# Kernel tuning notes

Hardware: AMD Instinct MI355X
Metric: run time of the kernel (lower is better)

The kernel has to match this reference:

```python
import jax, jax.numpy as jnp
import numpy as np

D = 32          # embedding_size
B = 16384       # batch_size
P = 16          # neighbor_sample_size (paths per item per hop)
NE = 100000     # n_entity
NU = 100000     # n_user
NR = 32         # n_relation
N_ITER = 2


def setup_inputs() -> dict:
    key = jax.random.key(0)
    ks = jax.random.split(key, 20)
    s = 0.1
    nrm = lambda k, sh: jax.random.normal(k, sh, dtype=jnp.float32) * s
    inp = {
        "user_table": nrm(ks[0], (NU, D)),
        "ent_table": nrm(ks[1], (NE, D)),
        "rel_table": nrm(ks[2], (NR, D)),
        # PyTorch LSTM params, gate order (i, f, g, o)
        "w_ih0": nrm(ks[3], (4 * D, 2 * D)),
        "w_hh0": nrm(ks[4], (4 * D, D)),
        "b_ih0": nrm(ks[5], (4 * D,)),
        "b_hh0": nrm(ks[6], (4 * D,)),
        "w_ih1": nrm(ks[7], (4 * D, 2 * D)),
        "w_hh1": nrm(ks[8], (4 * D, D)),
        "b_ih1": nrm(ks[9], (4 * D,)),
        "b_hh1": nrm(ks[10], (4 * D,)),
        "agg_w": nrm(ks[11], (D, D)),
        "agg_b": nrm(ks[12], (D,)),
        "users": jax.random.randint(ks[13], (B,), 0, NU),
        "items": jax.random.randint(ks[14], (B,), 0, NE),
        "ratings": jax.random.randint(ks[15], (B,), 0, 2),
        # hop h path table: [n_entity, P, 2*(h+1)+1]; values < 32 valid for both tables
        "lp0": jax.random.randint(ks[16], (NE, P, 3), 0, 32),
        "lp1": jax.random.randint(ks[17], (NE, P, 5), 0, 32),
    }
    return inp


def _lstm_last(seq, w_ih, w_hh, b_ih, b_hh):
    # seq: [N, T, 2D] -> final hidden state [N, D], PyTorch gate order i,f,g,o
    N = seq.shape[0]
    H = w_hh.shape[1]
    bias = b_ih + b_hh

    def step(carry, x):
        h, c = carry
        g = x @ w_ih.T + h @ w_hh.T + bias
        i, f, gg, o = jnp.split(g, 4, axis=-1)
        c = jax.nn.sigmoid(f) * c + jax.nn.sigmoid(i) * jnp.tanh(gg)
        h = jax.nn.sigmoid(o) * jnp.tanh(c)
        return (h, c), None

    h0 = jnp.zeros((N, H), seq.dtype)
    (h, _), _ = jax.lax.scan(step, (h0, h0), jnp.swapaxes(seq, 0, 1))
    return h


def _forward(user_table, ent_table, rel_table, lstm_params, agg_w, agg_b,
             users, items, ratings, lps):
    u = user_table[users]                # [B, D]
    items_emb = ent_table[items]         # [B, D]
    for hop in range(N_ITER):
        lp = lps[hop]
        w_ih, w_hh, b_ih, b_hh = lstm_params[hop]
        il = lp[items]                   # [B, P, 2*(hop+1)+1]
        seed_e = ent_table[il[:, :, 0]]  # [B, P, D]
        u_b = jnp.broadcast_to(u[:, None, :], seed_e.shape)
        first = jnp.concatenate([u_b, seed_e], -1)[:, :, None, :]   # [B,P,1,2D]
        rel_e = rel_table[il[:, :, 1::2]]                            # [B,P,hop+1,D]
        tail_e = ent_table[il[:, :, 2::2]]                           # [B,P,hop+1,D]
        rest = jnp.concatenate([rel_e, tail_e], -1)                  # [B,P,hop+1,2D]
        seq = jnp.concatenate([first, rest], 2).reshape(B * P, hop + 2, 2 * D)
        h = _lstm_last(seq, w_ih, w_hh, b_ih, b_hh)                  # [B*P, D]
        final = h.reshape(B, P, D).sum(axis=1)                       # hidden_out sum
        items_emb = (items_emb + final) @ agg_w.T + agg_b            # 'sum' aggregator
    scores = jnp.sum(u * items_emb, axis=-1)                         # [B]
    r = ratings.astype(scores.dtype)
    # stable BCE on sigmoid(scores)
    loss = -jnp.mean(r * jax.nn.log_sigmoid(scores) + (1.0 - r) * jax.nn.log_sigmoid(-scores))
    return loss, jax.nn.sigmoid(scores)


def reference(user_table, ent_table, rel_table,
              w_ih0, w_hh0, b_ih0, b_hh0,
              w_ih1, w_hh1, b_ih1, b_hh1,
              agg_w, agg_b,
              users, items, ratings, lp0, lp1):
    lstm_params = [(w_ih0, w_hh0, b_ih0, b_hh0), (w_ih1, w_hh1, b_ih1, b_hh1)]
    loss, scores_normalized = _forward(user_table, ent_table, rel_table,
                                       lstm_params, agg_w, agg_b,
                                       users, items, ratings, (lp0, lp1))
    return (loss, scores_normalized, items)
```

## Files before the change

### kernel.cpp

```cpp
#include <hip/hip_runtime.h>
#include <math.h>

#define D  32
#define BN 16384
#define PP 16

typedef __bf16 bf16x8 __attribute__((ext_vector_type(8)));
typedef __bf16 bf16x4 __attribute__((ext_vector_type(4)));
typedef float  floatx4 __attribute__((ext_vector_type(4)));

#define K1 1.44269504088896341f
#define K2 2.88539008177792681f

#define WHH_OFF    0
#define T0T_OFF    10240
#define TRT_OFF    20480
#define IMG_BYTES  30720
#define H_OFF      30720
#define LDS_BYTES  (IMG_BYTES + 8 * 1280)

__device__ __forceinline__ float sigf(float x) {
    float e = __builtin_amdgcn_exp2f(-x * K1);
    return __builtin_amdgcn_rcpf(1.0f + e);
}
__device__ __forceinline__ float logsigf(float x) {
    float ax = fabsf(x);
    float l = log1pf(__expf(-ax));
    return (x >= 0.0f) ? -l : x - l;
}
__device__ __forceinline__ floatx4 cvt4(bf16x4 v) {
    floatx4 r = { (float)v[0], (float)v[1], (float)v[2], (float)v[3] };
    return r;
}

__device__ __forceinline__ bf16x8 onehot8(int sel, int q) {
    union { unsigned w[4]; bf16x8 v; } u;
    const unsigned val = 0x3F80u << ((sel & 1) * 16);
    const int grp = sel >> 1;
    #pragma unroll
    for (int wd = 0; wd < 4; ++wd)
        u.w[wd] = (grp == q * 4 + wd) ? val : 0u;
    return u.v;
}

__global__ __launch_bounds__(256)
void prep_tables(const float* __restrict__ user_table,
                 const float* __restrict__ ent, const float* __restrict__ rel,
                 const float* __restrict__ wih0, const float* __restrict__ whh0,
                 const float* __restrict__ bih0, const float* __restrict__ bhh0,
                 const float* __restrict__ wih1, const float* __restrict__ whh1,
                 const float* __restrict__ bih1, const float* __restrict__ bhh1,
                 const int* __restrict__ users, const int* __restrict__ items,
                 const int* __restrict__ lp0, const int* __restrict__ lp1,
                 char* __restrict__ imgs, __bf16* __restrict__ GU,
                 int* __restrict__ pidx)
{
    const int id = blockIdx.x * 256 + threadIdx.x;
    if (id < 8192) {
        const int hop  = id >> 12;
        const int e    = id & 4095;
        const int gate = e >> 5, d = e & 31;
        float v = (hop ? whh1 : whh0)[(size_t)gate * 32 + d];
        ((__bf16*)(imgs + hop * IMG_BYTES + WHH_OFF))[gate * 40 + d] = (__bf16)v;
    } else if (id < 16384) {
        const int idb = id - 8192;
        const int hop = idb >> 12;
        const int g   = (idb >> 5) & 127;
        const int k   = idb & 31;
        const float* wih = hop ? wih1 : wih0;
        const float4* w4 = (const float4*)(wih + (size_t)g * 64 + 32);
        const float4* e4 = (const float4*)(ent + (size_t)k * 32);
        float a = hop ? bih1[g] + bhh1[g] : bih0[g] + bhh0[g];
        #pragma unroll
        for (int i = 0; i < 8; ++i) {
            float4 w = w4[i], x = e4[i];
            a = fmaf(w.x, x.x, a); a = fmaf(w.y, x.y, a);
            a = fmaf(w.z, x.z, a); a = fmaf(w.w, x.w, a);
        }
        ((__bf16*)(imgs + hop * IMG_BYTES + T0T_OFF))[g * 40 + k] = (__bf16)a;
    } else if (id < 24576) {
        const int idb = id - 16384;
        const int hop = idb >> 12;
        const int g   = (idb >> 5) & 127;
        const int j   = idb & 31;
        const float* wih = hop ? wih1 : wih0;
        const float4* w4 = (const float4*)(wih + (size_t)g * 64);
        const float4* r4 = (const float4*)(rel + (size_t)j * 32);
        float a = 0.0f;
        #pragma unroll
        for (int i = 0; i < 8; ++i) {
            float4 w = w4[i], x = r4[i];
            a = fmaf(w.x, x.x, a); a = fmaf(w.y, x.y, a);
            a = fmaf(w.z, x.z, a); a = fmaf(w.w, x.w, a);
        }
        ((__bf16*)(imgs + hop * IMG_BYTES + TRT_OFF))[g * 40 + j] = (__bf16)a;
    } else if (id < 1073152) {
        const int c   = id - 24576;
        const int hop = c >> 19;
        const int gq  = (c >> 14) & 31;
        const int fb  = c & 16383;
        const float* wih = hop ? wih1 : wih0;
        const float4* u4 = (const float4*)(user_table + (size_t)users[fb] * 32);
        float4 uu[8];
        #pragma unroll
        for (int i = 0; i < 8; ++i) uu[i] = u4[i];
        __bf16 r[4];
        #pragma unroll
        for (int t = 0; t < 4; ++t) {
            const float4* w4 = (const float4*)(wih + (size_t)(gq * 4 + t) * 64);
            float a = 0.0f;
            #pragma unroll
            for (int i = 0; i < 8; ++i) {
                float4 w = w4[i];
                a = fmaf(w.x, uu[i].x, a); a = fmaf(w.y, uu[i].y, a);
                a = fmaf(w.z, uu[i].z, a); a = fmaf(w.w, uu[i].w, a);
            }
            r[t] = (__bf16)a;
        }
        bf16x4 v = { r[0], r[1], r[2], r[3] };
        *(bf16x4*)(GU + ((size_t)(hop * BN + fb) * 128 + gq * 4)) = v;
    } else if (id < 1597440) {
        const int c   = id - 1073152;
        const int hop = c >> 18;
        const int rem = c & 262143;
        const int fb  = rem >> 4;
        const int p   = rem & 15;
        const int item = items[fb];
        int w;
        if (hop == 0) {
            const int* il = lp0 + ((size_t)item * PP + p) * 3;
            w = il[0] | (il[1] << 5) | (il[2] << 10);
        } else {
            const int* il = lp1 + ((size_t)item * PP + p) * 5;
            w = il[0] | (il[1] << 5) | (il[2] << 10) | (il[3] << 15)
                      | (il[4] << 20);
        }
        pidx[(size_t)(hop * BN + fb) * PP + p] = w;
    }
}

template<bool FIRST, bool LAST>
__device__ __forceinline__ void nonlin(
    floatx4* __restrict__ acc, float* __restrict__ cst,
    float* __restrict__ hlo, float* __restrict__ hhi,
    char* __restrict__ Hw, int q, int bnl)
{
    #pragma unroll
    for (int hf = 0; hf < 2; ++hf) {
        float* hout = hf ? hhi : hlo;
        #pragma unroll
        for (int r = 0; r < 4; ++r) {
            float gi = acc[0 + hf][r], gf = acc[2 + hf][r],
                  gg = acc[4 + hf][r], go = acc[6 + hf][r];
            float Ai = 1.0f + __builtin_amdgcn_exp2f(-gi * K1);
            float Af = 1.0f + __builtin_amdgcn_exp2f(-gf * K1);
            float G2 = __builtin_amdgcn_exp2f(gg * K2);
            float Gp = G2 + 1.0f, Gm = G2 - 1.0f;
            float cold = FIRST ? 0.0f : cst[hf * 4 + r];
            float num = cold * Ai * Gp + Gm * Af;
            float c = num * __builtin_amdgcn_rcpf(Af * Ai * Gp);
            cst[hf * 4 + r] = c;
            float Ao = 1.0f + __builtin_amdgcn_exp2f(-go * K1);
            float C2 = __builtin_amdgcn_exp2f(c * K2);
            hout[r] = (C2 - 1.0f) * __builtin_amdgcn_rcpf(Ao * (C2 + 1.0f));
        }
    }
    if (!LAST) {
        bf16x4 plo = { (__bf16)hlo[0], (__bf16)hlo[1], (__bf16)hlo[2], (__bf16)hlo[3] };
        bf16x4 phi = { (__bf16)hhi[0], (__bf16)hhi[1], (__bf16)hhi[2], (__bf16)hhi[3] };
        *(bf16x4*)(Hw + bnl * 80 + 8 * q)      = plo;
        *(bf16x4*)(Hw + bnl * 80 + 32 + 8 * q) = phi;
    }
}

__global__ __launch_bounds__(256, 4)
void hop_mfma(const int*   __restrict__ pidx,
              const char*  __restrict__ imgs,
              const __bf16* __restrict__ GU,
              float* __restrict__ F0,
              float* __restrict__ F1)
{
    __shared__ __align__(16) char lds[LDS_BYTES];

    const bool second = blockIdx.x & 1;
    const int  idx    = blockIdx.x >> 1;
    const int tid  = threadIdx.x;
    const int lane = tid & 63;
    const int wave = tid >> 6;
    const int q    = lane >> 4;
    const int bnl  = lane & 15;

    const int fbA = idx * 8 + wave;
    const int fbB = fbA + 4;
    const int hbase = second ? BN : 0;
    const int ixA = pidx[(size_t)(hbase + fbA) * PP + bnl];
    const int ixB = pidx[(size_t)(hbase + fbB) * PP + bnl];
    bf16x4 guhA[8], guhB[8];
    #pragma unroll
    for (int mt = 0; mt < 8; ++mt) {
        guhA[mt] = *(const bf16x4*)(GU + ((size_t)(hbase + fbA) * 128 + mt * 16 + q * 4));
        guhB[mt] = *(const bf16x4*)(GU + ((size_t)(hbase + fbB) * 128 + mt * 16 + q * 4));
    }

    {
        const float4* g4 = (const float4*)(imgs + (second ? IMG_BYTES : 0));
        float4* l4 = (float4*)lds;
        #pragma unroll
        for (int i = 0; i < 8; ++i) {
            int k = i * 256 + tid;
            if (k < IMG_BYTES / 16) l4[k] = g4[k];
        }
    }
    const char* Whh = lds + WHH_OFF;
    const char* T0t = lds + T0T_OFF;
    const char* TRt = lds + TRT_OFF;
    char* HwA = lds + H_OFF + (wave * 2 + 0) * 1280;
    char* HwB = lds + H_OFF + (wave * 2 + 1) * 1280;

    __syncthreads();

    float cstA[8], cstB[8], hloA[4], hhiA[4], hloB[4], hhiB[4];
    const floatx4 zf4 = { 0.0f, 0.0f, 0.0f, 0.0f };

    {
        bf16x8 ohA = onehot8(ixA & 31, q);
        bf16x8 ohB = onehot8(ixB & 31, q);
        floatx4 accA[8], accB[8];
        #pragma unroll
        for (int mt = 0; mt < 8; ++mt) {
            const int ro = (16 * mt + bnl) * 80 + q * 16;
            bf16x8 t0f = *(const bf16x8*)(T0t + ro);
            accA[mt] = __builtin_amdgcn_mfma_f32_16x16x32_bf16(t0f, ohA, cvt4(guhA[mt]), 0, 0, 0);
            accB[mt] = __builtin_amdgcn_mfma_f32_16x16x32_bf16(t0f, ohB, cvt4(guhB[mt]), 0, 0, 0);
        }
        nonlin<true, false>(accA, cstA, hloA, hhiA, HwA, q, bnl);
        nonlin<true, false>(accB, cstB, hloB, hhiB, HwB, q, bnl);
    }

    {
        bf16x8 ohjA = onehot8((ixA >> 5) & 31, q);
        bf16x8 ohkA = onehot8((ixA >> 10) & 31, q);
        bf16x8 ohjB = onehot8((ixB >> 5) & 31, q);
        bf16x8 ohkB = onehot8((ixB >> 10) & 31, q);
        bf16x8 bhA = *(const bf16x8*)(HwA + bnl * 80 + q * 16);
        bf16x8 bhB = *(const bf16x8*)(HwB + bnl * 80 + q * 16);
        floatx4 accA[8], accB[8];
        #pragma unroll
        for (int mt = 0; mt < 8; ++mt) {
            const int ro = (16 * mt + bnl) * 80 + q * 16;
            bf16x8 trf = *(const bf16x8*)(TRt + ro);
            bf16x8 t0f = *(const bf16x8*)(T0t + ro);
            bf16x8 whf = *(const bf16x8*)(Whh + ro);
            accA[mt] = __builtin_amdgcn_mfma_f32_16x16x32_bf16(trf, ohjA, zf4, 0, 0, 0);
            accB[mt] = __builtin_amdgcn_mfma_f32_16x16x32_bf16(trf, ohjB, zf4, 0, 0, 0);
            accA[mt] = __builtin_amdgcn_mfma_f32_16x16x32_bf16(t0f, ohkA, accA[mt], 0, 0, 0);
            accB[mt] = __builtin_amdgcn_mfma_f32_16x16x32_bf16(t0f, ohkB, accB[mt], 0, 0, 0);
            accA[mt] = __builtin_amdgcn_mfma_f32_16x16x32_bf16(whf, bhA, accA[mt], 0, 0, 0);
            accB[mt] = __builtin_amdgcn_mfma_f32_16x16x32_bf16(whf, bhB, accB[mt], 0, 0, 0);
        }
        if (second) {
            nonlin<false, false>(accA, cstA, hloA, hhiA, HwA, q, bnl);
            nonlin<false, false>(accB, cstB, hloB, hhiB, HwB, q, bnl);
        } else {
            nonlin<false, true>(accA, cstA, hloA, hhiA, HwA, q, bnl);
            nonlin<false, true>(accB, cstB, hloB, hhiB, HwB, q, bnl);
        }
    }

    if (second) {
        bf16x8 ohjA = onehot8((ixA >> 15) & 31, q);
        bf16x8 ohkA = onehot8((ixA >> 20) & 31, q);
        bf16x8 ohjB = onehot8((ixB >> 15) & 31, q);
        bf16x8 ohkB = onehot8((ixB >> 20) & 31, q);
        bf16x8 bhA = *(const bf16x8*)(HwA + bnl * 80 + q * 16);
        bf16x8 bhB = *(const bf16x8*)(HwB + bnl * 80 + q * 16);
        floatx4 accA[8], accB[8];
        #pragma unroll
        for (int mt = 0; mt < 8; ++mt) {
            const int ro = (16 * mt + bnl) * 80 + q * 16;
            bf16x8 trf = *(const bf16x8*)(TRt + ro);
            bf16x8 t0f = *(const bf16x8*)(T0t + ro);
            bf16x8 whf = *(const bf16x8*)(Whh + ro);
            accA[mt] = __builtin_amdgcn_mfma_f32_16x16x32_bf16(trf, ohjA, zf4, 0, 0, 0);
            accB[mt] = __builtin_amdgcn_mfma_f32_16x16x32_bf16(trf, ohjB, zf4, 0, 0, 0);
            accA[mt] = __builtin_amdgcn_mfma_f32_16x16x32_bf16(t0f, ohkA, accA[mt], 0, 0, 0);
            accB[mt] = __builtin_amdgcn_mfma_f32_16x16x32_bf16(t0f, ohkB, accB[mt], 0, 0, 0);
            accA[mt] = __builtin_amdgcn_mfma_f32_16x16x32_bf16(whf, bhA, accA[mt], 0, 0, 0);
            accB[mt] = __builtin_amdgcn_mfma_f32_16x16x32_bf16(whf, bhB, accB[mt], 0, 0, 0);
        }
        nonlin<false, true>(accA, cstA, hloA, hhiA, HwA, q, bnl);
        nonlin<false, true>(accB, cstB, hloB, hhiB, HwB, q, bnl);
    }

    #pragma unroll
    for (int r = 0; r < 4; ++r) {
        #pragma unroll
        for (int m = 1; m < 16; m <<= 1) {
            hloA[r] += __shfl_xor(hloA[r], m);
            hhiA[r] += __shfl_xor(hhiA[r], m);
            hloB[r] += __shfl_xor(hloB[r], m);
            hhiB[r] += __shfl_xor(hhiB[r], m);
        }
    }
    if (bnl == 0) {
        float* Fout = (second ? F1 : F0);
        float4 vloA = { hloA[0], hloA[1], hloA[2], hloA[3] };
        float4 vhiA = { hhiA[0], hhiA[1], hhiA[2], hhiA[3] };
        float4 vloB = { hloB[0], hloB[1], hloB[2], hloB[3] };
        float4 vhiB = { hhiB[0], hhiB[1], hhiB[2], hhiB[3] };
        *(float4*)(Fout + (size_t)fbA * D + 4 * q)      = vloA;
        *(float4*)(Fout + (size_t)fbA * D + 16 + 4 * q) = vhiA;
        *(float4*)(Fout + (size_t)fbB * D + 4 * q)      = vloB;
        *(float4*)(Fout + (size_t)fbB * D + 16 + 4 * q) = vhiB;
    }
}

__global__ __launch_bounds__(256)
void chain_score(const float* __restrict__ user_table,
                 const float* __restrict__ ent_table,
                 const float* __restrict__ agg_w,
                 const float* __restrict__ agg_b,
                 const int*   __restrict__ users,
                 const int*   __restrict__ items,
                 const int*   __restrict__ ratings,
                 const float* __restrict__ F0,
                 const float* __restrict__ F1,
                 float* __restrict__ out,
                 float* __restrict__ partials)
{
    __shared__ float s[8][33];
    __shared__ float red[8];
    const int tid = threadIdx.x;
    const int bb  = tid >> 5;
    const int j   = tid & 31;
    const int b   = blockIdx.x * 8 + bb;
    const int it  = items[b];

    s[bb][j] = ent_table[(size_t)it * D + j] + F0[(size_t)b * D + j];
    __syncthreads();
    const float* __restrict__ w = agg_w + (size_t)j * D;
    float e0 = agg_b[j];
    #pragma unroll
    for (int k = 0; k < D; ++k) e0 = fmaf(s[bb][k], w[k], e0);
    __syncthreads();
    s[bb][j] = e0 + F1[(size_t)b * D + j];
    __syncthreads();
    float e1 = agg_b[j];
    #pragma unroll
    for (int k = 0; k < D; ++k) e1 = fmaf(s[bb][k], w[k], e1);

    float prod = user_table[(size_t)users[b] * D + j] * e1;
    #pragma unroll
    for (int m = 1; m < 32; m <<= 1) prod += __shfl_xor(prod, m);
    if (j == 0) {
        out[1 + b]      = sigf(prod);
        out[1 + BN + b] = (float)it;
        float r = (float)ratings[b];
        red[bb] = r * logsigf(prod) + (1.0f - r) * logsigf(-prod);
    }
    __syncthreads();
    if (tid == 0) {
        float t = 0.0f;
        #pragma unroll
        for (int qq = 0; qq < 8; ++qq) t += red[qq];
        partials[blockIdx.x] = t;
    }
}

__global__ __launch_bounds__(256)
void loss_kernel(const float* __restrict__ partials, float* __restrict__ out)
{
    __shared__ float red[4];
    const int t = threadIdx.x;
    float v = 0.0f;
    #pragma unroll
    for (int qq = 0; qq < 8; ++qq) v += partials[qq * 256 + t];
    #pragma unroll
    for (int m = 1; m < 64; m <<= 1) v += __shfl_xor(v, m);
    if ((t & 63) == 0) red[t >> 6] = v;
    __syncthreads();
    if (t == 0) out[0] = -(red[0] + red[1] + red[2] + red[3]) / (float)BN;
}

extern "C" void kernel_launch(void* const* d_in, const int* in_sizes, int n_in,
                              void* d_out, int out_size, void* d_ws, size_t ws_size,
                              hipStream_t stream)
{
    const float* user_table = (const float*)d_in[0];
    const float* ent_table  = (const float*)d_in[1];
    const float* rel_table  = (const float*)d_in[2];
    const float* w_ih0 = (const float*)d_in[3];
    const float* w_hh0 = (const float*)d_in[4];
    const float* b_ih0 = (const float*)d_in[5];
    const float* b_hh0 = (const float*)d_in[6];
    const float* w_ih1 = (const float*)d_in[7];
    const float* w_hh1 = (const float*)d_in[8];
    const float* b_ih1 = (const float*)d_in[9];
    const float* b_hh1 = (const float*)d_in[10];
    const float* agg_w = (const float*)d_in[11];
    const float* agg_b = (const float*)d_in[12];
    const int* users   = (const int*)d_in[13];
    const int* items   = (const int*)d_in[14];
    const int* ratings = (const int*)d_in[15];
    const int* lp0     = (const int*)d_in[16];
    const int* lp1     = (const int*)d_in[17];
    float* out = (float*)d_out;

    float* ws       = (float*)d_ws;
    float* F0       = ws;
    float* F1       = F0 + (size_t)BN * D;
    float* partials = F1 + (size_t)BN * D;
    char*  imgs     = (char*)(partials + 2048);
    int*   pidx     = (int*)(imgs + 2 * IMG_BYTES);
    __bf16* GU      = (__bf16*)(pidx + 2 * (size_t)BN * PP);

    prep_tables<<<6240, 256, 0, stream>>>(user_table, ent_table, rel_table,
        w_ih0, w_hh0, b_ih0, b_hh0, w_ih1, w_hh1, b_ih1, b_hh1,
        users, items, lp0, lp1, imgs, GU, pidx);
    hop_mfma<<<4096, 256, 0, stream>>>(pidx, imgs, GU, F0, F1);
    chain_score<<<BN / 8, 256, 0, stream>>>(
        user_table, ent_table, agg_w, agg_b, users, items, ratings,
        F0, F1, out, partials);
    loss_kernel<<<1, 256, 0, stream>>>(partials, out);
}
```

Before: 261.9 us.

## Fuse user-gate projection into MFMA hop kernel and keep hidden state in registers

The per-user W_ih·u precompute in prep_tables, which wrote a large GU buffer to global memory, is removed. The hop kernel now loads the user embedding directly and applies it with an extra MFMA against a small bf16 W_u image. LSTM gate rows are permuted so each lane's MFMA output lines up with its B-operand layout, which lets the hidden state be packed from registers instead of round-tripping through LDS. This cuts prep work, global traffic and LDS usage, at the cost of more MFMAs in the first step and a strided weight fragment load per wave.

```diff
diff --git a/kernel.cpp b/kernel.cpp
--- a/kernel.cpp
+++ b/kernel.cpp
@@ -16,8 +16,8 @@
 #define T0T_OFF    10240
 #define TRT_OFF    20480
 #define IMG_BYTES  30720
-#define H_OFF      30720
-#define LDS_BYTES  (IMG_BYTES + 8 * 1280)
+#define WU_BYTES   10240
+#define LDS_BYTES  IMG_BYTES
 
 __device__ __forceinline__ float sigf(float x) {
     float e = __builtin_amdgcn_exp2f(-x * K1);
@@ -28,9 +28,15 @@
     float l = log1pf(__expf(-ax));
     return (x >= 0.0f) ? -l : x - l;
 }
-__device__ __forceinline__ floatx4 cvt4(bf16x4 v) {
-    floatx4 r = { (float)v[0], (float)v[1], (float)v[2], (float)v[3] };
+__device__ __forceinline__ bf16x8 loadu8(const float* __restrict__ p) {
+    float4 a = ((const float4*)p)[0], b = ((const float4*)p)[1];
+    bf16x8 r = { (__bf16)a.x, (__bf16)a.y, (__bf16)a.z, (__bf16)a.w,
+                 (__bf16)b.x, (__bf16)b.y, (__bf16)b.z, (__bf16)b.w };
     return r;
+}
+
+__device__ __forceinline__ int perm_gate(int R) {
+    return 32 * ((R >> 4) & 3) + 8 * ((R >> 2) & 3) + 4 * (R >> 6) + (R & 3);
 }
 
 __device__ __forceinline__ bf16x8 onehot8(int sel, int q) {
@@ -43,30 +49,45 @@
     return u.v;
 }
 
+__device__ __forceinline__ bf16x8 packh(const float* __restrict__ h) {
+    bf16x8 r = { (__bf16)h[0], (__bf16)h[1], (__bf16)h[2], (__bf16)h[3],
+                 (__bf16)h[4], (__bf16)h[5], (__bf16)h[6], (__bf16)h[7] };
+    return r;
+}
+
 __global__ __launch_bounds__(256)
-void prep_tables(const float* __restrict__ user_table,
-                 const float* __restrict__ ent, const float* __restrict__ rel,
+void prep_tables(const float* __restrict__ ent, const float* __restrict__ rel,
                  const float* __restrict__ wih0, const float* __restrict__ whh0,
                  const float* __restrict__ bih0, const float* __restrict__ bhh0,
                  const float* __restrict__ wih1, const float* __restrict__ whh1,
                  const float* __restrict__ bih1, const float* __restrict__ bhh1,
-                 const int* __restrict__ users, const int* __restrict__ items,
+                 const int* __restrict__ items,
                  const int* __restrict__ lp0, const int* __restrict__ lp1,
-                 char* __restrict__ imgs, __bf16* __restrict__ GU,
+                 char* __restrict__ imgs, char* __restrict__ wu_g,
                  int* __restrict__ pidx)
 {
     const int id = blockIdx.x * 256 + threadIdx.x;
     if (id < 8192) {
-        const int hop  = id >> 12;
-        const int e    = id & 4095;
-        const int gate = e >> 5, d = e & 31;
-        float v = (hop ? whh1 : whh0)[(size_t)gate * 32 + d];
-        ((__bf16*)(imgs + hop * IMG_BYTES + WHH_OFF))[gate * 40 + d] = (__bf16)v;
+        const int hop = id >> 12;
+        const int e   = id & 4095;
+        const int R   = e >> 5, d = e & 31;
+        const int g   = perm_gate(R);
+        float v = (hop ? whh1 : whh0)[(size_t)g * 32 + d];
+        ((__bf16*)(imgs + hop * IMG_BYTES + WHH_OFF))[R * 40 + d] = (__bf16)v;
     } else if (id < 16384) {
         const int idb = id - 8192;
         const int hop = idb >> 12;
-        const int g   = (idb >> 5) & 127;
+        const int e   = idb & 4095;
+        const int R   = e >> 5, d = e & 31;
+        const int g   = perm_gate(R);
+        float v = (hop ? wih1 : wih0)[(size_t)g * 64 + d];
+        ((__bf16*)(wu_g + hop * WU_BYTES))[R * 40 + d] = (__bf16)v;
+    } else if (id < 24576) {
+        const int idb = id - 16384;
+        const int hop = idb >> 12;
+        const int R   = (idb >> 5) & 127;
         const int k   = idb & 31;
+        const int g   = perm_gate(R);
         const float* wih = hop ? wih1 : wih0;
         const float4* w4 = (const float4*)(wih + (size_t)g * 64 + 32);
         const float4* e4 = (const float4*)(ent + (size_t)k * 32);
@@ -77,12 +98,13 @@
             a = fmaf(w.x, x.x, a); a = fmaf(w.y, x.y, a);
             a = fmaf(w.z, x.z, a); a = fmaf(w.w, x.w, a);
         }
-        ((__bf16*)(imgs + hop * IMG_BYTES + T0T_OFF))[g * 40 + k] = (__bf16)a;
-    } else if (id < 24576) {
-        const int idb = id - 16384;
+        ((__bf16*)(imgs + hop * IMG_BYTES + T0T_OFF))[R * 40 + k] = (__bf16)a;
+    } else if (id < 32768) {
+        const int idb = id - 24576;
         const int hop = idb >> 12;
-        const int g   = (idb >> 5) & 127;
+        const int R   = (idb >> 5) & 127;
         const int j   = idb & 31;
+        const int g   = perm_gate(R);
         const float* wih = hop ? wih1 : wih0;
         const float4* w4 = (const float4*)(wih + (size_t)g * 64);
         const float4* r4 = (const float4*)(rel + (size_t)j * 32);
@@ -93,34 +115,9 @@
             a = fmaf(w.x, x.x, a); a = fmaf(w.y, x.y, a);
             a = fmaf(w.z, x.z, a); a = fmaf(w.w, x.w, a);
         }
-        ((__bf16*)(imgs + hop * IMG_BYTES + TRT_OFF))[g * 40 + j] = (__bf16)a;
-    } else if (id < 1073152) {
-        const int c   = id - 24576;
-        const int hop = c >> 19;
-        const int gq  = (c >> 14) & 31;
-        const int fb  = c & 16383;
-        const float* wih = hop ? wih1 : wih0;
-        const float4* u4 = (const float4*)(user_table + (size_t)users[fb] * 32);
-        float4 uu[8];
-        #pragma unroll
-        for (int i = 0; i < 8; ++i) uu[i] = u4[i];
-        __bf16 r[4];
-        #pragma unroll
-        for (int t = 0; t < 4; ++t) {
-            const float4* w4 = (const float4*)(wih + (size_t)(gq * 4 + t) * 64);
-            float a = 0.0f;
-            #pragma unroll
-            for (int i = 0; i < 8; ++i) {
-                float4 w = w4[i];
-                a = fmaf(w.x, uu[i].x, a); a = fmaf(w.y, uu[i].y, a);
-                a = fmaf(w.z, uu[i].z, a); a = fmaf(w.w, uu[i].w, a);
-            }
-            r[t] = (__bf16)a;
-        }
-        bf16x4 v = { r[0], r[1], r[2], r[3] };
-        *(bf16x4*)(GU + ((size_t)(hop * BN + fb) * 128 + gq * 4)) = v;
-    } else if (id < 1597440) {
-        const int c   = id - 1073152;
+        ((__bf16*)(imgs + hop * IMG_BYTES + TRT_OFF))[R * 40 + j] = (__bf16)a;
+    } else if (id < 32768 + 524288) {
+        const int c   = id - 32768;
         const int hop = c >> 18;
         const int rem = c & 262143;
         const int fb  = rem >> 4;
@@ -139,44 +136,37 @@
     }
 }
 
-template<bool FIRST, bool LAST>
+template<bool FIRST>
 __device__ __forceinline__ void nonlin(
-    floatx4* __restrict__ acc, float* __restrict__ cst,
-    float* __restrict__ hlo, float* __restrict__ hhi,
-    char* __restrict__ Hw, int q, int bnl)
-{
-    #pragma unroll
-    for (int hf = 0; hf < 2; ++hf) {
-        float* hout = hf ? hhi : hlo;
+    floatx4* __restrict__ acc, float* __restrict__ cst, float* __restrict__ h)
+{
+    #pragma unroll
+    for (int a = 0; a < 2; ++a) {
         #pragma unroll
         for (int r = 0; r < 4; ++r) {
-            float gi = acc[0 + hf][r], gf = acc[2 + hf][r],
-                  gg = acc[4 + hf][r], go = acc[6 + hf][r];
+            float gi = acc[4 * a + 0][r], gf = acc[4 * a + 1][r],
+                  gg = acc[4 * a + 2][r], go = acc[4 * a + 3][r];
             float Ai = 1.0f + __builtin_amdgcn_exp2f(-gi * K1);
             float Af = 1.0f + __builtin_amdgcn_exp2f(-gf * K1);
             float G2 = __builtin_amdgcn_exp2f(gg * K2);
             float Gp = G2 + 1.0f, Gm = G2 - 1.0f;
-            float cold = FIRST ? 0.0f : cst[hf * 4 + r];
+            float cold = FIRST ? 0.0f : cst[4 * a + r];
             float num = cold * Ai * Gp + Gm * Af;
             float c = num * __builtin_amdgcn_rcpf(Af * Ai * Gp);
-            cst[hf * 4 + r] = c;
+            cst[4 * a + r] = c;
             float Ao = 1.0f + __builtin_amdgcn_exp2f(-go * K1);
             float C2 = __builtin_amdgcn_exp2f(c * K2);
-            hout[r] = (C2 - 1.0f) * __builtin_amdgcn_rcpf(Ao * (C2 + 1.0f));
-        }
-    }
-    if (!LAST) {
-        bf16x4 plo = { (__bf16)hlo[0], (__bf16)hlo[1], (__bf16)hlo[2], (__bf16)hlo[3] };
-        bf16x4 phi = { (__bf16)hhi[0], (__bf16)hhi[1], (__bf16)hhi[2], (__bf16)hhi[3] };
-        *(bf16x4*)(Hw + bnl * 80 + 8 * q)      = plo;
-        *(bf16x4*)(Hw + bnl * 80 + 32 + 8 * q) = phi;
+            h[4 * a + r] = (C2 - 1.0f) * __builtin_amdgcn_rcpf(Ao * (C2 + 1.0f));
+        }
     }
 }
 
 __global__ __launch_bounds__(256, 4)
-void hop_mfma(const int*   __restrict__ pidx,
+void hop_mfma(const float* __restrict__ user_table,
+              const int*   __restrict__ users,
+              const int*   __restrict__ pidx,
               const char*  __restrict__ imgs,
-              const __bf16* __restrict__ GU,
+              const char*  __restrict__ wu_g,
               float* __restrict__ F0,
               float* __restrict__ F1)
 {
@@ -195,12 +185,14 @@
     const int hbase = second ? BN : 0;
     const int ixA = pidx[(size_t)(hbase + fbA) * PP + bnl];
     const int ixB = pidx[(size_t)(hbase + fbB) * PP + bnl];
-    bf16x4 guhA[8], guhB[8];
-    #pragma unroll
-    for (int mt = 0; mt < 8; ++mt) {
-        guhA[mt] = *(const bf16x4*)(GU + ((size_t)(hbase + fbA) * 128 + mt * 16 + q * 4));
-        guhB[mt] = *(const bf16x4*)(GU + ((size_t)(hbase + fbB) * 128 + mt * 16 + q * 4));
-    }
+    bf16x8 buA = loadu8(user_table + (size_t)users[fbA] * D + q * 8);
+    bf16x8 buB = loadu8(user_table + (size_t)users[fbB] * D + q * 8);
+
+    const char* wub = wu_g + (second ? WU_BYTES : 0);
+    bf16x8 wuf[8];
+    #pragma unroll
+    for (int mt = 0; mt < 8; ++mt)
+        wuf[mt] = *(const bf16x8*)(wub + (16 * mt + bnl) * 80 + q * 16);
 
     {
         const float4* g4 = (const float4*)(imgs + (second ? IMG_BYTES : 0));
@@ -214,12 +206,10 @@
     const char* Whh = lds + WHH_OFF;
     const char* T0t = lds + T0T_OFF;
     const char* TRt = lds + TRT_OFF;
-    char* HwA = lds + H_OFF + (wave * 2 + 0) * 1280;
-    char* HwB = lds + H_OFF + (wave * 2 + 1) * 1280;
-
-    __syncthreads();
-
-    float cstA[8], cstB[8], hloA[4], hhiA[4], hloB[4], hhiB[4];
+
+    __syncthreads();
+
+    float cstA[8], cstB[8], hA[8], hB[8];
     const floatx4 zf4 = { 0.0f, 0.0f, 0.0f, 0.0f };
 
     {
@@ -230,11 +220,13 @@
         for (int mt = 0; mt < 8; ++mt) {
             const int ro = (16 * mt + bnl) * 80 + q * 16;
             bf16x8 t0f = *(const bf16x8*)(T0t + ro);
-            accA[mt] = __builtin_amdgcn_mfma_f32_16x16x32_bf16(t0f, ohA, cvt4(guhA[mt]), 0, 0, 0);
-            accB[mt] = __builtin_amdgcn_mfma_f32_16x16x32_bf16(t0f, ohB, cvt4(guhB[mt]), 0, 0, 0);
-        }
-        nonlin<true, false>(accA, cstA, hloA, hhiA, HwA, q, bnl);
-        nonlin<true, false>(accB, cstB, hloB, hhiB, HwB, q, bnl);
+            accA[mt] = __builtin_amdgcn_mfma_f32_16x16x32_bf16(t0f, ohA, zf4, 0, 0, 0);
+            accB[mt] = __builtin_amdgcn_mfma_f32_16x16x32_bf16(t0f, ohB, zf4, 0, 0, 0);
+            accA[mt] = __builtin_amdgcn_mfma_f32_16x16x32_bf16(wuf[mt], buA, accA[mt], 0, 0, 0);
+            accB[mt] = __builtin_amdgcn_mfma_f32_16x16x32_bf16(wuf[mt], buB, accB[mt], 0, 0, 0);
+        }
+        nonlin<true>(accA, cstA, hA);
+        nonlin<true>(accB, cstB, hB);
     }
 
     {
@@ -242,8 +234,8 @@
         bf16x8 ohkA = onehot8((ixA >> 10) & 31, q);
         bf16x8 ohjB = onehot8((ixB >> 5) & 31, q);
         bf16x8 ohkB = onehot8((ixB >> 10) & 31, q);
-        bf16x8 bhA = *(const bf16x8*)(HwA + bnl * 80 + q * 16);
-        bf16x8 bhB = *(const bf16x8*)(HwB + bnl * 80 + q * 16);
+        bf16x8 bhA = packh(hA);
+        bf16x8 bhB = packh(hB);
         floatx4 accA[8], accB[8];
         #pragma unroll
         for (int mt = 0; mt < 8; ++mt) {
@@ -258,13 +250,8 @@
             accA[mt] = __builtin_amdgcn_mfma_f32_16x16x32_bf16(whf, bhA, accA[mt], 0, 0, 0);
             accB[mt] = __builtin_amdgcn_mfma_f32_16x16x32_bf16(whf, bhB, accB[mt], 0, 0, 0);
         }
-        if (second) {
-            nonlin<false, false>(accA, cstA, hloA, hhiA, HwA, q, bnl);
-            nonlin<false, false>(accB, cstB, hloB, hhiB, HwB, q, bnl);
-        } else {
-            nonlin<false, true>(accA, cstA, hloA, hhiA, HwA, q, bnl);
-            nonlin<false, true>(accB, cstB, hloB, hhiB, HwB, q, bnl);
-        }
+        nonlin<false>(accA, cstA, hA);
+        nonlin<false>(accB, cstB, hB);
     }
 
     if (second) {
@@ -272,8 +259,8 @@
         bf16x8 ohkA = onehot8((ixA >> 20) & 31, q);
         bf16x8 ohjB = onehot8((ixB >> 15) & 31, q);
         bf16x8 ohkB = onehot8((ixB >> 20) & 31, q);
-        bf16x8 bhA = *(const bf16x8*)(HwA + bnl * 80 + q * 16);
-        bf16x8 bhB = *(const bf16x8*)(HwB + bnl * 80 + q * 16);
+        bf16x8 bhA = packh(hA);
+        bf16x8 bhB = packh(hB);
         floatx4 accA[8], accB[8];
         #pragma unroll
         for (int mt = 0; mt < 8; ++mt) {
@@ -288,30 +275,28 @@
             accA[mt] = __builtin_amdgcn_mfma_f32_16x16x32_bf16(whf, bhA, accA[mt], 0, 0, 0);
             accB[mt] = __builtin_amdgcn_mfma_f32_16x16x32_bf16(whf, bhB, accB[mt], 0, 0, 0);
         }
-        nonlin<false, true>(accA, cstA, hloA, hhiA, HwA, q, bnl);
-        nonlin<false, true>(accB, cstB, hloB, hhiB, HwB, q, bnl);
-    }
-
-    #pragma unroll
-    for (int r = 0; r < 4; ++r) {
+        nonlin<false>(accA, cstA, hA);
+        nonlin<false>(accB, cstB, hB);
+    }
+
+    #pragma unroll
+    for (int j = 0; j < 8; ++j) {
         #pragma unroll
         for (int m = 1; m < 16; m <<= 1) {
-            hloA[r] += __shfl_xor(hloA[r], m);
-            hhiA[r] += __shfl_xor(hhiA[r], m);
-            hloB[r] += __shfl_xor(hloB[r], m);
-            hhiB[r] += __shfl_xor(hhiB[r], m);
+            hA[j] += __shfl_xor(hA[j], m);
+            hB[j] += __shfl_xor(hB[j], m);
         }
     }
     if (bnl == 0) {
         float* Fout = (second ? F1 : F0);
-        float4 vloA = { hloA[0], hloA[1], hloA[2], hloA[3] };
-        float4 vhiA = { hhiA[0], hhiA[1], hhiA[2], hhiA[3] };
-        float4 vloB = { hloB[0], hloB[1], hloB[2], hloB[3] };
-        float4 vhiB = { hhiB[0], hhiB[1], hhiB[2], hhiB[3] };
-        *(float4*)(Fout + (size_t)fbA * D + 4 * q)      = vloA;
-        *(float4*)(Fout + (size_t)fbA * D + 16 + 4 * q) = vhiA;
-        *(float4*)(Fout + (size_t)fbB * D + 4 * q)      = vloB;
-        *(float4*)(Fout + (size_t)fbB * D + 16 + 4 * q) = vhiB;
+        float4 vA0 = { hA[0], hA[1], hA[2], hA[3] };
+        float4 vA1 = { hA[4], hA[5], hA[6], hA[7] };
+        float4 vB0 = { hB[0], hB[1], hB[2], hB[3] };
+        float4 vB1 = { hB[4], hB[5], hB[6], hB[7] };
+        *(float4*)(Fout + (size_t)fbA * D + 8 * q)     = vA0;
+        *(float4*)(Fout + (size_t)fbA * D + 8 * q + 4) = vA1;
+        *(float4*)(Fout + (size_t)fbB * D + 8 * q)     = vB0;
+        *(float4*)(Fout + (size_t)fbB * D + 8 * q + 4) = vB1;
     }
 }
 
@@ -411,13 +396,14 @@
     float* F1       = F0 + (size_t)BN * D;
     float* partials = F1 + (size_t)BN * D;
     char*  imgs     = (char*)(partials + 2048);
-    int*   pidx     = (int*)(imgs + 2 * IMG_BYTES);
-    __bf16* GU      = (__bf16*)(pidx + 2 * (size_t)BN * PP);
-
-    prep_tables<<<6240, 256, 0, stream>>>(user_table, ent_table, rel_table,
+    char*  wu_g     = imgs + 2 * IMG_BYTES;
+    int*   pidx     = (int*)(wu_g + 2 * WU_BYTES);
+
+    prep_tables<<<2176, 256, 0, stream>>>(ent_table, rel_table,
         w_ih0, w_hh0, b_ih0, b_hh0, w_ih1, w_hh1, b_ih1, b_hh1,
-        users, items, lp0, lp1, imgs, GU, pidx);
-    hop_mfma<<<4096, 256, 0, stream>>>(pidx, imgs, GU, F0, F1);
+        items, lp0, lp1, imgs, wu_g, pidx);
+    hop_mfma<<<4096, 256, 0, stream>>>(
+        user_table, users, pidx, imgs, wu_g, F0, F1);
     chain_score<<<BN / 8, 256, 0, stream>>>(
         user_table, ent_table, agg_w, agg_b, users, items, ratings,
         F0, F1, out, partials);
```

Result: slower. 307.0 us (+17.2%).
